# Optimization experiments

Hardware: AMD Instinct MI355X
Metric: run time of the kernel (lower is better)

Reference implementation:

```python
import jax, jax.numpy as jnp
import numpy as np

C = 512
NC = 12
EPS = 1e-5

ADJ = np.array([
    [0,0,0,1,0,1,1,1,1,1,1,1],
    [0,0,0,1,0,1,1,1,1,1,1,1],
    [0,0,0,1,0,1,1,1,1,1,1,1],
    [1,1,1,0,1,1,1,1,1,1,1,1],
    [0,0,0,1,0,1,1,1,1,1,1,1],
    [1,1,1,1,1,0,1,1,1,0,0,0],
    [1,1,1,1,1,1,0,0,0,1,1,1],
    [1,1,1,1,1,1,0,0,0,1,1,1],
    [1,1,1,1,1,1,0,0,0,1,1,1],
    [1,1,1,1,1,0,1,1,1,0,0,0],
    [1,1,1,1,1,0,1,1,1,0,0,0],
    [1,1,1,1,1,0,1,1,1,0,0,0]], dtype=np.float32)
# per-AU region selection: 0=up,1=mid,2=down1,3=down2 (AU1,2,4 up; AU6 mid; AU7 up; AU10 d2; AU12,14,15 d1; AU17,23,24 d2)
SEL = np.array([0,0,0,1,0,3,2,2,2,3,3,3])


def setup_inputs() -> dict:
    key = jax.random.key(0)
    ks = jax.random.split(key, 12)
    B, T = 32, 32
    BT = B * T
    s = (2.0 / C) ** 0.5
    return {
        'x': jax.random.normal(ks[0], (BT, 49, C), jnp.float32),
        'adj_mask': jnp.ones((BT, NC, NC), jnp.float32),
        'region_W': jax.random.normal(ks[1], (4, C, C), jnp.float32) * s,
        'region_b': jnp.zeros((4, C), jnp.float32),
        'region_gamma': jnp.ones((4, C), jnp.float32),
        'region_beta': jnp.zeros((4, C), jnp.float32),
        'upfc_W': jax.random.normal(ks[2], (C, 16), jnp.float32) * 0.02,
        'upfc_b': jnp.zeros((16,), jnp.float32),
        'midfc_W': jax.random.normal(ks[3], (C, 2), jnp.float32) * 0.02,
        'midfc_b': jnp.zeros((2,), jnp.float32),
        'd1fc_W': jax.random.normal(ks[4], (C, 8), jnp.float32) * 0.02,
        'd1fc_b': jnp.zeros((8,), jnp.float32),
        'd2fc_W': jax.random.normal(ks[5], (C, 16), jnp.float32) * 0.02,
        'd2fc_b': jnp.zeros((16,), jnp.float32),
        'class_W': jax.random.normal(ks[6], (NC, C, C), jnp.float32) * s,
        'class_b': jnp.zeros((NC, C), jnp.float32),
        'class_gamma': jnp.ones((NC, C), jnp.float32),
        'class_beta': jnp.zeros((NC, C), jnp.float32),
        'gat_W': jax.random.normal(ks[7], (C, C), jnp.float32) * 0.02,
        'gat_al': jax.random.normal(ks[8], (C,), jnp.float32) * 0.02,
        'gat_ar': jax.random.normal(ks[9], (C,), jnp.float32) * 0.02,
        'tconv_W': jax.random.normal(ks[10], (NC, C, 5), jnp.float32) * 0.1,
        'tconv_b': jnp.zeros((NC, C), jnp.float32),
        'tbn_gamma': jnp.ones((NC,), jnp.float32),
        'tbn_beta': jnp.zeros((NC,), jnp.float32),
        'B': B,
        'T': T,
    }


def _bn(x, gamma, beta, axes):
    # training-mode batch norm: stats over `axes`, affine per remaining channel
    mean = x.mean(axes, keepdims=True)
    var = x.var(axes, keepdims=True)
    return gamma * (x - mean) * jax.lax.rsqrt(var + EPS) + beta


def reference(x, adj_mask, region_W, region_b, region_gamma, region_beta,
              upfc_W, upfc_b, midfc_W, midfc_b, d1fc_W, d1fc_b, d2fc_W, d2fc_b,
              class_W, class_b, class_gamma, class_beta,
              gat_W, gat_al, gat_ar, tconv_W, tconv_b, tbn_gamma, tbn_beta, B, T):
    BT = x.shape[0]
    xg = x.reshape(BT, 7, 7, C)
    x_up = xg[:, :3].reshape(BT, 21, C)
    x_mid = xg[:, 2:5].reshape(BT, 21, C)
    x_down = xg[:, 4:].reshape(BT, 21, C)
    # 4 region LinearBlocks (fc -> BN over (batch,seq) per channel -> relu), batched
    regions = jnp.stack([x_up, x_mid, x_down, x_down])  # [4,BT,21,C]
    h = jnp.einsum('rbsc,rcd->rbsd', regions, region_W) + region_b[:, None, None, :]
    h = jax.nn.relu(_bn(h, region_gamma[:, None, None, :], region_beta[:, None, None, :], (1, 2)))
    up_pred = h[0].mean(1) @ upfc_W + upfc_b
    mid_pred = h[1].mean(1) @ midfc_W + midfc_b
    d1_pred = h[2].mean(1) @ d1fc_W + d1fc_b
    d2_pred = h[3].mean(1) @ d2fc_W + d2fc_b
    # 12 per-AU LinearBlocks, batched over the class dim
    cls_in = h[jnp.asarray(SEL)]  # [12,BT,21,C]
    y = jnp.einsum('nbsc,ncd->nbsd', cls_in, class_W) + class_b[:, None, None, :]
    y = jax.nn.relu(_bn(y, class_gamma[:, None, None, :], class_beta[:, None, None, :], (1, 2)))
    f_v = y.mean(2).transpose(1, 0, 2)  # [BT,12,C]
    # cross-region single-head GAT over the fixed 12-node graph, residual, thred=0.1
    adj = jnp.asarray(ADJ)[None] * adj_mask + jnp.eye(NC, dtype=x.dtype)
    hg = f_v @ gat_W  # [BT,12,C]
    e = jax.nn.leaky_relu((hg @ gat_al)[:, :, None] + (hg @ gat_ar)[:, None, :], 0.2)
    attn = jax.nn.softmax(jnp.where(adj > 0.1, e, -1e9), axis=-1)
    g = jnp.einsum('bij,bjc->bic', attn, hg) + f_v
    # per-class depthwise temporal Conv1d (k=5, pad=2, groups=C), batched over classes
    x4 = g.reshape(B, T, NC, C)
    xp = jnp.pad(x4, ((0, 0), (2, 2), (0, 0), (0, 0)))
    v = sum(xp[:, k:k + T] * tconv_W[None, None, :, :, k] for k in range(5)) + tconv_b[None, None]
    v = v.reshape(BT, NC, C)
    out = jax.nn.relu(_bn(v, tbn_gamma[None, :, None], tbn_beta[None, :, None], (0, 2)))
    return (up_pred, mid_pred, d1_pred, d2_pred, out)
```

## Files before the change

### kernel.cpp

```cpp
#include <hip/hip_runtime.h>
#include <hip/hip_bf16.h>

typedef unsigned short u16;
typedef __attribute__((ext_vector_type(8))) __bf16 bf16x8;
typedef __attribute__((ext_vector_type(8))) u16 u16x8;
typedef __attribute__((ext_vector_type(4))) float floatx4;

#define C_     512
#define NC_    12
#define BT_    1024
#define SEQ_   21
#define M_REG  21504
#define M_GAT  12288

__device__ __forceinline__ float bf2f(u16 u) {
  unsigned int v = ((unsigned int)u) << 16;
  float f; __builtin_memcpy(&f, &v, 4); return f;
}
__device__ __forceinline__ u16 f2bf(float f) {
  unsigned int b; __builtin_memcpy(&b, &f, 4);
  unsigned int r = (b + 0x7FFFu + ((b >> 16) & 1u)) >> 16;
  return (u16)r;
}
__device__ __forceinline__ float ldf(const void* p, size_t i, int f32) {
  return f32 ? ((const float*)p)[i] : bf2f(((const u16*)p)[i]);
}
__device__ __forceinline__ u16 ldbf(const void* p, size_t i, int f32) {
  return f32 ? f2bf(((const float*)p)[i]) : ((const u16*)p)[i];
}
__device__ __forceinline__ void stout(void* p, size_t i, float v, int f32) {
  if (f32) ((float*)p)[i] = v; else ((u16*)p)[i] = f2bf(v);
}

__global__ void sent_k(float* __restrict__ o, float val) {
  const int i = blockIdx.x * 256 + threadIdx.x;
  if (i < 16384) o[i] = val;
}

__global__ void detect_k(const u16* __restrict__ x, int* __restrict__ flag) {
  __shared__ int cnt;
  if (threadIdx.x == 0) cnt = 0;
  __syncthreads();
  int bad = 0;
  for (int i = threadIdx.x; i < 4096; i += 256) {
    const float v = bf2f(x[i]);
    const float a = fabsf(v);
    if (!(a <= 1e4f)) bad++;
    else if (a > 0.f && a < 1e-35f) bad++;
  }
  atomicAdd(&cnt, bad);
  __syncthreads();
  if (threadIdx.x == 0) *flag = (cnt > 400) ? 1 : 0;
}

__global__ void zero_stats(float* __restrict__ p, int n) {
  const int id = blockIdx.x * 256 + threadIdx.x;
  if (id < n) p[id] = 0.f;
}

__global__ void transpose512(const void* __restrict__ rW, const void* __restrict__ cW,
                             const void* __restrict__ gW, u16* __restrict__ oR,
                             u16* __restrict__ oC, u16* __restrict__ oG,
                             const int* __restrict__ flagp) {
  const int f32 = *flagp;
  const int z = blockIdx.z;
  const void* src; u16* dst; size_t sofs = 0;
  if (z < 4)       { src = rW; sofs = (size_t)z*262144;     dst = oR + (size_t)z*262144; }
  else if (z < 16) { src = cW; sofs = (size_t)(z-4)*262144; dst = oC + (size_t)(z-4)*262144; }
  else             { src = gW;                              dst = oG; }
  __shared__ u16 t[32][33];
  const int tx = threadIdx.x;
  const int cy = blockIdx.y * 32, dx = blockIdx.x * 32;
  for (int i = threadIdx.y; i < 32; i += 8)
    t[i][tx] = ldbf(src, sofs + (size_t)(cy + i)*512 + dx + tx, f32);
  __syncthreads();
  for (int i = threadIdx.y; i < 32; i += 8)
    dst[(size_t)(dx + i)*512 + cy + tx] = t[tx][i];
}

template<int MODE>
__global__ __launch_bounds__(256)
void gemm_k(const void* __restrict__ Abase, const u16* __restrict__ Wtb,
            const void* __restrict__ biasb, u16* __restrict__ outb,
            float* __restrict__ ssumb, float* __restrict__ ssqb,
            const int* __restrict__ flagp, int pk, int n0)
{
  const int f32 = *flagp;
  const int z = blockIdx.z;
  const int zeff = (MODE == 1) ? (n0 + z) : z;
  const void* A = Abase;
  if (MODE == 1) A = (const void*)((const u16*)Abase +
        (size_t)((pk >> (zeff * 2)) & 3) * ((size_t)M_REG * C_));
  const u16* Wt = Wtb + (size_t)zeff * C_ * C_;
  u16* Out = outb + (size_t)z * (size_t)M_REG * C_;

  __shared__ __align__(16) u16 As[128*32];
  __shared__ __align__(16) u16 Bs[128*32];

  const int tid  = threadIdx.x;
  const int w    = tid >> 6;
  const int lane = tid & 63;
  const int wm   = w >> 1, wn = w & 1;
  const int r16  = lane & 15, q = lane >> 4;

  const int m0  = blockIdx.y * 128;
  const int nn0 = blockIdx.x * 128;

  const int sub = lane >> 2;
  const int kq  = (lane & 3) * 8;
  const int am0 = m0 + w*32 + sub;
  const int am1 = am0 + 16;
  long ga0, ga1;
  if (MODE == 0) {
    const int roff = (pk >> (z * 8)) & 0xFF;
    int q21 = am0 / 21; int rm = am0 - q21*21;
    ga0 = (long)q21*49 + roff + rm;
    q21 = am1 / 21; rm = am1 - q21*21;
    ga1 = (long)q21*49 + roff + rm;
  } else { ga0 = am0; ga1 = am1; }
  const size_t aOff0 = (size_t)ga0 * C_ + kq;
  const size_t aOff1 = (size_t)ga1 * C_ + kq;
  const u16* bSrc0 = Wt + (size_t)(nn0 + w*32 + sub) * C_ + kq;
  const u16* bSrc1 = bSrc0 + (size_t)16 * C_;
  u16x8* aLds0 = (u16x8*)&As[(w*32 + sub +  0) * 32 + kq];
  u16x8* aLds1 = (u16x8*)&As[(w*32 + sub + 16) * 32 + kq];
  u16x8* bLds0 = (u16x8*)&Bs[(w*32 + sub +  0) * 32 + kq];
  u16x8* bLds1 = (u16x8*)&Bs[(w*32 + sub + 16) * 32 + kq];

  floatx4 acc[4][4];
  #pragma unroll
  for (int i = 0; i < 4; i++)
    #pragma unroll
    for (int j = 0; j < 4; j++)
      acc[i][j] = (floatx4){0.f, 0.f, 0.f, 0.f};

  for (int kk = 0; kk < C_; kk += 32) {
    u16x8 va0, va1;
    if (MODE == 0 && f32) {
      const float* p0 = (const float*)A + aOff0 + kk;
      const float* p1 = (const float*)A + aOff1 + kk;
      const floatx4 f00 = *(const floatx4*)p0;
      const floatx4 f01 = *(const floatx4*)(p0 + 4);
      const floatx4 f10 = *(const floatx4*)p1;
      const floatx4 f11 = *(const floatx4*)(p1 + 4);
      #pragma unroll
      for (int j = 0; j < 4; j++) {
        va0[j] = f2bf(f00[j]); va0[4+j] = f2bf(f01[j]);
        va1[j] = f2bf(f10[j]); va1[4+j] = f2bf(f11[j]);
      }
    } else {
      va0 = *(const u16x8*)((const u16*)A + aOff0 + kk);
      va1 = *(const u16x8*)((const u16*)A + aOff1 + kk);
    }
    const u16x8 vb0 = *(const u16x8*)bSrc0;
    const u16x8 vb1 = *(const u16x8*)bSrc1;
    bSrc0 += 32; bSrc1 += 32;
    __syncthreads();
    *aLds0 = va0; *aLds1 = va1; *bLds0 = vb0; *bLds1 = vb1;
    __syncthreads();
    bf16x8 av[4], bv[4];
    #pragma unroll
    for (int mt = 0; mt < 4; mt++)
      av[mt] = *(const bf16x8*)&As[(wm*64 + mt*16 + r16)*32 + q*8];
    #pragma unroll
    for (int nt = 0; nt < 4; nt++)
      bv[nt] = *(const bf16x8*)&Bs[(wn*64 + nt*16 + r16)*32 + q*8];
    #pragma unroll
    for (int mt = 0; mt < 4; mt++)
      #pragma unroll
      for (int nt = 0; nt < 4; nt++)
        acc[mt][nt] = __builtin_amdgcn_mfma_f32_16x16x32_bf16(av[mt], bv[nt], acc[mt][nt], 0, 0, 0);
  }

  const int colb = nn0 + wn*64;
  const int rowb = m0  + wm*64;
  #pragma unroll
  for (int nt = 0; nt < 4; nt++) {
    const int col = colb + nt*16 + r16;
    float bvv = 0.f;
    if (MODE != 2) bvv = ldf(biasb, (size_t)zeff * C_ + col, f32);
    float s = 0.f, s2 = 0.f;
    #pragma unroll
    for (int mt = 0; mt < 4; mt++) {
      #pragma unroll
      for (int p = 0; p < 4; p++) {
        float v = acc[mt][nt][p] + bvv;
        const int row = rowb + mt*16 + q*4 + p;
        Out[(size_t)row * C_ + col] = f2bf(v);
        s += v; s2 += v*v;
      }
    }
    if (MODE != 2) {
      s  += __shfl_xor(s, 16);  s  += __shfl_xor(s, 32);
      s2 += __shfl_xor(s2, 16); s2 += __shfl_xor(s2, 32);
      if (q == 0) {
        atomicAdd(&ssumb[(size_t)zeff * C_ + col], s);
        atomicAdd(&ssqb [(size_t)zeff * C_ + col], s2);
      }
    }
  }
}

__global__ void bn_region(u16* __restrict__ h, float* __restrict__ hbar,
                          const void* __restrict__ gamma, const void* __restrict__ beta,
                          const float* __restrict__ rsum, const float* __restrict__ rsq,
                          const int* __restrict__ flagp) {
  const int f32 = *flagp;
  const size_t id = (size_t)blockIdx.x * 256 + threadIdx.x;
  const int d  = (int)(id & 511);
  const int bt = (int)((id >> 9) & 1023);
  const int r  = (int)(id >> 19);
  const int rd = r*512 + d;
  const float mean = rsum[rd] * (1.f/21504.f);
  const float var  = fmaxf(rsq[rd] * (1.f/21504.f) - mean*mean, 0.f);
  const float sc = ldf(gamma, rd, f32) * rsqrtf(var + 1e-5f);
  const float sh = ldf(beta, rd, f32) - mean * sc;
  const size_t base = ((size_t)r * M_REG + (size_t)bt * SEQ_) * C_ + d;
  float acc = 0.f;
  #pragma unroll
  for (int s = 0; s < SEQ_; s++) {
    float v = fmaxf(sc * bf2f(h[base + (size_t)s*C_]) + sh, 0.f);
    h[base + (size_t)s*C_] = f2bf(v);
    acc += v;
  }
  hbar[((size_t)r * BT_ + bt) * C_ + d] = acc * (1.f/21.f);
}

__global__ void preds_k(const float* __restrict__ hbar,
                        const void* __restrict__ upW,  const void* __restrict__ upB,
                        const void* __restrict__ midW, const void* __restrict__ midB,
                        const void* __restrict__ d1W,  const void* __restrict__ d1B,
                        const void* __restrict__ d2W,  const void* __restrict__ d2B,
                        void* __restrict__ dout, const int* __restrict__ flagp) {
  const int f32 = *flagp;
  const int bt = blockIdx.x;
  __shared__ float hl[4][512];
  for (int i = threadIdx.x; i < 2048; i += 256)
    hl[i >> 9][i & 511] = hbar[((size_t)(i >> 9) * BT_ + bt) * C_ + (i & 511)];
  __syncthreads();
  const int j = threadIdx.x;
  if (j < 42) {
    int r, wdt, col; const void *W, *Bv; size_t oofs;
    if (j < 16)      { r=0; W=upW;  Bv=upB;  wdt=16; col=j;    oofs = (size_t)bt*16 + col; }
    else if (j < 18) { r=1; W=midW; Bv=midB; wdt=2;  col=j-16; oofs = 16384 + (size_t)bt*2 + col; }
    else if (j < 26) { r=2; W=d1W;  Bv=d1B;  wdt=8;  col=j-18; oofs = 18432 + (size_t)bt*8 + col; }
    else             { r=3; W=d2W;  Bv=d2B;  wdt=16; col=j-26; oofs = 26624 + (size_t)bt*16 + col; }
    float acc = ldf(Bv, col, f32);
    for (int d = 0; d < 512; d++) acc += hl[r][d] * ldf(W, d*wdt + col, f32);
    stout(dout, oofs, acc, f32);
  }
}

__global__ void bn_class_mean(const u16* __restrict__ ypre, u16* __restrict__ fv,
                              const void* __restrict__ gamma, const void* __restrict__ beta,
                              const float* __restrict__ csum, const float* __restrict__ csq,
                              const int* __restrict__ flagp, int n0) {
  const int f32 = *flagp;
  const size_t id = (size_t)blockIdx.x * 256 + threadIdx.x;
  const int d  = (int)(id & 511);
  const int bt = (int)((id >> 9) & 1023);
  const int zz = (int)(id >> 19);
  const int n  = n0 + zz;
  const int nd = n*512 + d;
  const float mean = csum[nd] * (1.f/21504.f);
  const float var  = fmaxf(csq[nd] * (1.f/21504.f) - mean*mean, 0.f);
  const float sc = ldf(gamma, nd, f32) * rsqrtf(var + 1e-5f);
  const float sh = ldf(beta, nd, f32) - mean * sc;
  const size_t base = ((size_t)zz * M_REG + (size_t)bt * SEQ_) * C_ + d;
  float acc = 0.f;
  #pragma unroll
  for (int s = 0; s < SEQ_; s++)
    acc += fmaxf(sc * bf2f(ypre[base + (size_t)s*C_]) + sh, 0.f);
  fv[((size_t)bt * NC_ + n) * C_ + d] = f2bf(acc * (1.f/21.f));
}

__global__ __launch_bounds__(256)
void gat_k(const u16* __restrict__ hg, const u16* __restrict__ fv,
           const void* __restrict__ al, const void* __restrict__ ar,
           const void* __restrict__ adj_mask, float* __restrict__ g,
           const int* __restrict__ flagp) {
  const int f32 = *flagp;
  const int bt = blockIdx.x;
  __shared__ float hl[12][512];
  __shared__ float alv[12], arv[12], attn[12][12];
  const u16* hgb = hg + (size_t)bt * NC_ * C_;
  for (int i = threadIdx.x; i < 6144; i += 256)
    hl[i >> 9][i & 511] = bf2f(hgb[i]);
  __syncthreads();
  const int w = threadIdx.x >> 6, lane = threadIdx.x & 63;
  for (int i = w; i < 12; i += 4) {
    float pa = 0.f, pr = 0.f;
    #pragma unroll
    for (int jj = 0; jj < 8; jj++) {
      const int c = lane*8 + jj;
      const float hv = hl[i][c];
      pa += hv * ldf(al, c, f32);
      pr += hv * ldf(ar, c, f32);
    }
    #pragma unroll
    for (int off = 32; off; off >>= 1) { pa += __shfl_xor(pa, off); pr += __shfl_xor(pr, off); }
    if (lane == 0) { alv[i] = pa; arv[i] = pr; }
  }
  __syncthreads();
  if (threadIdx.x < 12) {
    const unsigned AM[12] = {0xFE8,0xFE8,0xFE8,0xFF7,0xFE8,0x1DF,
                             0xE3F,0xE3F,0xE3F,0x1DF,0x1DF,0x1DF};
    const int i = threadIdx.x;
    float row[12]; float mx = -1e30f;
    #pragma unroll
    for (int jx = 0; jx < 12; jx++) {
      const float maskv = ldf(adj_mask, (size_t)bt*144 + i*12 + jx, f32);
      const float adjv = (float)((AM[i] >> jx) & 1u) * maskv + (i == jx ? 1.f : 0.f);
      float e;
      if (adjv > 0.1f) {
        const float t = alv[i] + arv[jx];
        e = t > 0.f ? t : 0.2f * t;
      } else e = -1e9f;
      row[jx] = e; mx = fmaxf(mx, e);
    }
    float den = 0.f;
    #pragma unroll
    for (int jx = 0; jx < 12; jx++) { const float ex = __expf(row[jx] - mx); row[jx] = ex; den += ex; }
    const float inv = 1.f / den;
    #pragma unroll
    for (int jx = 0; jx < 12; jx++) attn[i][jx] = row[jx] * inv;
  }
  __syncthreads();
  const u16* fvb = fv + (size_t)bt * NC_ * C_;
  float* gb = g + (size_t)bt * NC_ * C_;
  for (int o = threadIdx.x; o < 6144; o += 256) {
    const int i = o >> 9, c = o & 511;
    float acc = bf2f(fvb[o]);
    #pragma unroll
    for (int jx = 0; jx < 12; jx++) acc += attn[i][jx] * hl[jx][c];
    gb[o] = acc;
  }
}

__global__ void tconv_k(float* __restrict__ g, const void* __restrict__ tw,
                        const void* __restrict__ tb, float* __restrict__ tsum,
                        float* __restrict__ tsq, const int* __restrict__ flagp) {
  const int f32 = *flagp;
  const int id = blockIdx.x * 256 + threadIdx.x;
  const int c = id & 511;
  const int n = (id >> 9) % 12;
  const int b = id / 6144;
  float wk[5];
  #pragma unroll
  for (int k = 0; k < 5; k++) wk[k] = ldf(tw, (size_t)(n*512 + c)*5 + k, f32);
  const float bias = ldf(tb, n*512 + c, f32);
  float xv[36];
  xv[0] = xv[1] = xv[34] = xv[35] = 0.f;
  const size_t base = ((size_t)b * 32 * NC_ + n) * C_ + c;
  #pragma unroll
  for (int t = 0; t < 32; t++) xv[t + 2] = g[base + (size_t)t * 6144];
  float s = 0.f, s2 = 0.f;
  float ov[32];
  #pragma unroll
  for (int t = 0; t < 32; t++) {
    float v = bias;
    #pragma unroll
    for (int k = 0; k < 5; k++) v += wk[k] * xv[t + k];
    ov[t] = v; s += v; s2 += v*v;
  }
  #pragma unroll
  for (int t = 0; t < 32; t++) g[base + (size_t)t * 6144] = ov[t];
  #pragma unroll
  for (int off = 32; off; off >>= 1) { s += __shfl_xor(s, off); s2 += __shfl_xor(s2, off); }
  if ((threadIdx.x & 63) == 0) { atomicAdd(&tsum[n], s); atomicAdd(&tsq[n], s2); }
}

__global__ void bn_t(const float* __restrict__ v, void* __restrict__ outp,
                     const void* __restrict__ tg, const void* __restrict__ tb2,
                     const float* __restrict__ tsum, const float* __restrict__ tsq,
                     const int* __restrict__ flagp) {
  const int f32 = *flagp;
  const size_t id = (size_t)blockIdx.x * 256 + threadIdx.x;
  const int n = (int)((id >> 9) % 12);
  const float mean = tsum[n] * (1.f/524288.f);
  const float var  = fmaxf(tsq[n] * (1.f/524288.f) - mean*mean, 0.f);
  const float sc = ldf(tg, n, f32) * rsqrtf(var + 1e-5f);
  const float sh = ldf(tb2, n, f32) - mean * sc;
  stout(outp, 43008 + id, fmaxf(sc * v[id] + sh, 0.f), f32);
}

static constexpr size_t OFF_FLAG = 0;
static constexpr size_t OFF_STAT = 64;
static constexpr int    STAT_N   = 2048+2048+6144+6144+12+12;
static constexpr size_t OFF_WTR  = 65792;
static constexpr size_t OFF_WTC  = OFF_WTR + (size_t)4*512*512*2;
static constexpr size_t OFF_WTG  = OFF_WTC + (size_t)12*512*512*2;
static constexpr size_t OFF_H    = OFF_WTG + (size_t)512*512*2;
static constexpr size_t OFF_HBAR = OFF_H + (size_t)4*M_REG*C_*2;
static constexpr size_t OFF_FV   = OFF_HBAR + (size_t)4*BT_*C_*4;
static constexpr size_t OFF_AREN = OFF_FV + (size_t)M_GAT*C_*2;
static constexpr size_t YPRE_B   = (size_t)M_REG * C_ * 2;
static constexpr size_t NEEDED   = OFF_AREN + YPRE_B;

extern "C" void kernel_launch(void* const* d_in, const int* in_sizes, int n_in,
                              void* d_out, int out_size, void* d_ws, size_t ws_size,
                              hipStream_t stream) {
  const u16* x        = (const u16*)d_in[0];
  const void* adj_m   = d_in[1];
  const void* region_W= d_in[2];
  const void* region_b= d_in[3];
  const void* region_g= d_in[4];
  const void* region_be=d_in[5];
  const void* upW  = d_in[6];   const void* upB  = d_in[7];
  const void* midW = d_in[8];   const void* midB = d_in[9];
  const void* d1W  = d_in[10];  const void* d1B  = d_in[11];
  const void* d2W  = d_in[12];  const void* d2B  = d_in[13];
  const void* class_W = d_in[14];
  const void* class_b = d_in[15];
  const void* class_g = d_in[16];
  const void* class_be= d_in[17];
  const void* gat_W   = d_in[18];
  const void* gat_al  = d_in[19];
  const void* gat_ar  = d_in[20];
  const void* tconv_W = d_in[21];
  const void* tconv_b = d_in[22];
  const void* tbn_g   = d_in[23];
  const void* tbn_be  = d_in[24];

  char* ws = (char*)d_ws;
  int*   flagp = (int*)(ws + OFF_FLAG);
  float* rsum = (float*)(ws + OFF_STAT);
  float* rsq  = rsum + 2048;
  float* csum = rsq  + 2048;
  float* csq  = csum + 6144;
  float* tsum = csq  + 6144;
  float* tsq  = tsum + 12;
  u16*   WtR  = (u16*)(ws + OFF_WTR);
  u16*   WtC  = (u16*)(ws + OFF_WTC);
  u16*   WtG  = (u16*)(ws + OFF_WTG);
  u16*   h    = (u16*)(ws + OFF_H);
  float* hbar = (float*)(ws + OFF_HBAR);
  u16*   fv   = (u16*)(ws + OFF_FV);
  u16*   ypre = (u16*)(ws + OFF_AREN);
  u16*   hg   = (u16*)(ws + OFF_AREN);
  float* g    = (float*)(ws + OFF_H);

  int errStage = 0, errCode = 0;
  (void)hipGetLastError();
  #define CK(s) do { hipError_t e_ = hipGetLastError(); \
      if (e_ != hipSuccess && errStage == 0) { errStage = (s); errCode = (int)e_; } } while(0)

  sent_k<<<64, 256, 0, stream>>>((float*)d_out, 50.f); CK(12);

  if (ws_size < NEEDED) {
    int mb = (int)(ws_size >> 20); if (mb > 999) mb = 999;
    sent_k<<<64, 256, 0, stream>>>((float*)d_out, 13000.f + (float)mb);
    return;
  }

  int nch = (int)((ws_size - OFF_AREN) / YPRE_B);
  if (nch > 12) nch = 12;
  if (nch < 1) nch = 1;

  const int ROFFPACK = 0 | (14 << 8) | (28 << 16) | (28 << 24);
  const int SELPACK  = (1 << 6) | (3 << 10) | (2 << 12) | (2 << 14) |
                       (2 << 16) | (3 << 18) | (3 << 20) | (3 << 22);

  detect_k<<<1, 256, 0, stream>>>(x, flagp);                         CK(1);
  zero_stats<<<(STAT_N + 255)/256, 256, 0, stream>>>(rsum, STAT_N);  CK(1);
  transpose512<<<dim3(16,16,17), dim3(32,8), 0, stream>>>(
      region_W, class_W, gat_W, WtR, WtC, WtG, flagp);               CK(2);

  gemm_k<0><<<dim3(4,168,4), 256, 0, stream>>>(
      x, WtR, region_b, h, rsum, rsq, flagp, ROFFPACK, 0);           CK(3);
  bn_region<<<8192, 256, 0, stream>>>(h, hbar, region_g, region_be,
      rsum, rsq, flagp);                                             CK(4);
  preds_k<<<1024, 256, 0, stream>>>(hbar, upW,upB, midW,midB,
      d1W,d1B, d2W,d2B, d_out, flagp);                               CK(5);

  for (int n0 = 0; n0 < 12; n0 += nch) {
    const int zc = (12 - n0) < nch ? (12 - n0) : nch;
    gemm_k<1><<<dim3(4,168,zc), 256, 0, stream>>>(
        h, WtC - (size_t)n0*262144 + (size_t)n0*262144, class_b, ypre,
        csum, csq, flagp, SELPACK, n0);                              CK(6);
    bn_class_mean<<<zc*2048, 256, 0, stream>>>(ypre, fv, class_g, class_be,
        csum, csq, flagp, n0);                                       CK(7);
  }

  gemm_k<2><<<dim3(4,96,1), 256, 0, stream>>>(
      fv, WtG, nullptr, hg, nullptr, nullptr, flagp, 0, 0);          CK(8);
  gat_k<<<1024, 256, 0, stream>>>(hg, fv, gat_al, gat_ar, adj_m, g, flagp); CK(9);
  tconv_k<<<768, 256, 0, stream>>>(g, tconv_W, tconv_b, tsum, tsq, flagp);  CK(10);
  bn_t<<<24576, 256, 0, stream>>>(g, d_out, tbn_g, tbn_be, tsum, tsq, flagp); CK(11);

  if (errStage) {
    int ec = errCode > 999 ? 999 : errCode;
    sent_k<<<64, 256, 0, stream>>>((float*)d_out, (float)(errStage*1000 + ec));
  }
  #undef CK
}
```

Measured before the change: 894.1 us.

## Use direct global-to-LDS loads in GEMM and vectorize BN reduction kernels

The GEMM tile loads now use global_load_lds to copy A and B tiles straight into shared memory instead of staging them through registers. The f32 path keeps its register conversion for A and uses the direct path only for B. The bn_region and bn_class_mean kernels now have each lane handle 8 contiguous channels with 16-byte vector loads and stores, using one-eighth as many blocks. This cuts register traffic and instruction count in memory-bound kernels. The risk is that the LDS layout written by global_load_lds must match the old per-lane write pattern, and per-thread register use rises in the BN kernels.

```diff
diff --git a/kernel.cpp b/kernel.cpp
--- a/kernel.cpp
+++ b/kernel.cpp
@@ -30,6 +30,12 @@
 }
 __device__ __forceinline__ void stout(void* p, size_t i, float v, int f32) {
   if (f32) ((float*)p)[i] = v; else ((u16*)p)[i] = f2bf(v);
+}
+
+typedef __attribute__((address_space(1))) unsigned int as1_u32;
+typedef __attribute__((address_space(3))) unsigned int as3_u32;
+__device__ __forceinline__ void gl2lds16(const void* g, void* l) {
+  __builtin_amdgcn_global_load_lds((const as1_u32*)g, (as3_u32*)l, 16, 0, 0);
 }
 
 __global__ void sent_k(float* __restrict__ o, float val) {
@@ -122,10 +128,12 @@
   const size_t aOff1 = (size_t)ga1 * C_ + kq;
   const u16* bSrc0 = Wt + (size_t)(nn0 + w*32 + sub) * C_ + kq;
   const u16* bSrc1 = bSrc0 + (size_t)16 * C_;
+  u16* aDstW0 = &As[(w*32 +  0) * 32];
+  u16* aDstW1 = &As[(w*32 + 16) * 32];
+  u16* bDstW0 = &Bs[(w*32 +  0) * 32];
+  u16* bDstW1 = &Bs[(w*32 + 16) * 32];
   u16x8* aLds0 = (u16x8*)&As[(w*32 + sub +  0) * 32 + kq];
   u16x8* aLds1 = (u16x8*)&As[(w*32 + sub + 16) * 32 + kq];
-  u16x8* bLds0 = (u16x8*)&Bs[(w*32 + sub +  0) * 32 + kq];
-  u16x8* bLds1 = (u16x8*)&Bs[(w*32 + sub + 16) * 32 + kq];
 
   floatx4 acc[4][4];
   #pragma unroll
@@ -135,7 +143,6 @@
       acc[i][j] = (floatx4){0.f, 0.f, 0.f, 0.f};
 
   for (int kk = 0; kk < C_; kk += 32) {
-    u16x8 va0, va1;
     if (MODE == 0 && f32) {
       const float* p0 = (const float*)A + aOff0 + kk;
       const float* p1 = (const float*)A + aOff1 + kk;
@@ -143,21 +150,25 @@
       const floatx4 f01 = *(const floatx4*)(p0 + 4);
       const floatx4 f10 = *(const floatx4*)p1;
       const floatx4 f11 = *(const floatx4*)(p1 + 4);
+      u16x8 va0, va1;
       #pragma unroll
       for (int j = 0; j < 4; j++) {
         va0[j] = f2bf(f00[j]); va0[4+j] = f2bf(f01[j]);
         va1[j] = f2bf(f10[j]); va1[4+j] = f2bf(f11[j]);
       }
+      __syncthreads();
+      gl2lds16(bSrc0, bDstW0); gl2lds16(bSrc1, bDstW1);
+      *aLds0 = va0; *aLds1 = va1;
+      __syncthreads();
     } else {
-      va0 = *(const u16x8*)((const u16*)A + aOff0 + kk);
-      va1 = *(const u16x8*)((const u16*)A + aOff1 + kk);
+      __syncthreads();
+      gl2lds16((const u16*)A + aOff0 + kk, aDstW0);
+      gl2lds16((const u16*)A + aOff1 + kk, aDstW1);
+      gl2lds16(bSrc0, bDstW0);
+      gl2lds16(bSrc1, bDstW1);
+      __syncthreads();
     }
-    const u16x8 vb0 = *(const u16x8*)bSrc0;
-    const u16x8 vb1 = *(const u16x8*)bSrc1;
     bSrc0 += 32; bSrc1 += 32;
-    __syncthreads();
-    *aLds0 = va0; *aLds1 = va1; *bLds0 = vb0; *bLds1 = vb1;
-    __syncthreads();
     bf16x8 av[4], bv[4];
     #pragma unroll
     for (int mt = 0; mt < 4; mt++)
@@ -206,24 +217,36 @@
                           const float* __restrict__ rsum, const float* __restrict__ rsq,
                           const int* __restrict__ flagp) {
   const int f32 = *flagp;
-  const size_t id = (size_t)blockIdx.x * 256 + threadIdx.x;
-  const int d  = (int)(id & 511);
-  const int bt = (int)((id >> 9) & 1023);
-  const int r  = (int)(id >> 19);
-  const int rd = r*512 + d;
-  const float mean = rsum[rd] * (1.f/21504.f);
-  const float var  = fmaxf(rsq[rd] * (1.f/21504.f) - mean*mean, 0.f);
-  const float sc = ldf(gamma, rd, f32) * rsqrtf(var + 1e-5f);
-  const float sh = ldf(beta, rd, f32) - mean * sc;
-  const size_t base = ((size_t)r * M_REG + (size_t)bt * SEQ_) * C_ + d;
-  float acc = 0.f;
+  const int gid  = blockIdx.x;
+  const int r    = gid >> 8;
+  const int bt   = ((gid & 255) << 2) + (threadIdx.x >> 6);
+  const int lane = threadIdx.x & 63;
+  const int d0   = lane * 8;
+  const int rd   = r*512 + d0;
+  float sc[8], sh[8], accv[8];
+  #pragma unroll
+  for (int j = 0; j < 8; j++) {
+    const float mean = rsum[rd+j] * (1.f/21504.f);
+    const float var  = fmaxf(rsq[rd+j] * (1.f/21504.f) - mean*mean, 0.f);
+    sc[j] = ldf(gamma, rd+j, f32) * rsqrtf(var + 1e-5f);
+    sh[j] = ldf(beta,  rd+j, f32) - mean * sc[j];
+    accv[j] = 0.f;
+  }
+  const size_t base = ((size_t)r * M_REG + (size_t)bt * SEQ_) * C_ + d0;
   #pragma unroll
   for (int s = 0; s < SEQ_; s++) {
-    float v = fmaxf(sc * bf2f(h[base + (size_t)s*C_]) + sh, 0.f);
-    h[base + (size_t)s*C_] = f2bf(v);
-    acc += v;
-  }
-  hbar[((size_t)r * BT_ + bt) * C_ + d] = acc * (1.f/21.f);
+    u16x8 vv = *(u16x8*)&h[base + (size_t)s*C_];
+    #pragma unroll
+    for (int j = 0; j < 8; j++) {
+      float v = fmaxf(sc[j] * bf2f(vv[j]) + sh[j], 0.f);
+      vv[j] = f2bf(v);
+      accv[j] += v;
+    }
+    *(u16x8*)&h[base + (size_t)s*C_] = vv;
+  }
+  float* hb = &hbar[((size_t)r * BT_ + bt) * C_ + d0];
+  #pragma unroll
+  for (int j = 0; j < 8; j++) hb[j] = accv[j] * (1.f/21.f);
 }
 
 __global__ void preds_k(const float* __restrict__ hbar,
@@ -256,22 +279,34 @@
                               const float* __restrict__ csum, const float* __restrict__ csq,
                               const int* __restrict__ flagp, int n0) {
   const int f32 = *flagp;
-  const size_t id = (size_t)blockIdx.x * 256 + threadIdx.x;
-  const int d  = (int)(id & 511);
-  const int bt = (int)((id >> 9) & 1023);
-  const int zz = (int)(id >> 19);
-  const int n  = n0 + zz;
-  const int nd = n*512 + d;
-  const float mean = csum[nd] * (1.f/21504.f);
-  const float var  = fmaxf(csq[nd] * (1.f/21504.f) - mean*mean, 0.f);
-  const float sc = ldf(gamma, nd, f32) * rsqrtf(var + 1e-5f);
-  const float sh = ldf(beta, nd, f32) - mean * sc;
-  const size_t base = ((size_t)zz * M_REG + (size_t)bt * SEQ_) * C_ + d;
-  float acc = 0.f;
-  #pragma unroll
-  for (int s = 0; s < SEQ_; s++)
-    acc += fmaxf(sc * bf2f(ypre[base + (size_t)s*C_]) + sh, 0.f);
-  fv[((size_t)bt * NC_ + n) * C_ + d] = f2bf(acc * (1.f/21.f));
+  const int gid  = blockIdx.x;
+  const int zz   = gid >> 8;
+  const int bt   = ((gid & 255) << 2) + (threadIdx.x >> 6);
+  const int lane = threadIdx.x & 63;
+  const int d0   = lane * 8;
+  const int n    = n0 + zz;
+  const int nd   = n*512 + d0;
+  float sc[8], sh[8], accv[8];
+  #pragma unroll
+  for (int j = 0; j < 8; j++) {
+    const float mean = csum[nd+j] * (1.f/21504.f);
+    const float var  = fmaxf(csq[nd+j] * (1.f/21504.f) - mean*mean, 0.f);
+    sc[j] = ldf(gamma, nd+j, f32) * rsqrtf(var + 1e-5f);
+    sh[j] = ldf(beta,  nd+j, f32) - mean * sc[j];
+    accv[j] = 0.f;
+  }
+  const size_t base = ((size_t)zz * M_REG + (size_t)bt * SEQ_) * C_ + d0;
+  #pragma unroll
+  for (int s = 0; s < SEQ_; s++) {
+    const u16x8 vv = *(const u16x8*)&ypre[base + (size_t)s*C_];
+    #pragma unroll
+    for (int j = 0; j < 8; j++)
+      accv[j] += fmaxf(sc[j] * bf2f(vv[j]) + sh[j], 0.f);
+  }
+  u16x8 ov;
+  #pragma unroll
+  for (int j = 0; j < 8; j++) ov[j] = f2bf(accv[j] * (1.f/21.f));
+  *(u16x8*)&fv[((size_t)bt * NC_ + n) * C_ + d0] = ov;
 }
 
 __global__ __launch_bounds__(256)
@@ -468,7 +503,7 @@
 
   gemm_k<0><<<dim3(4,168,4), 256, 0, stream>>>(
       x, WtR, region_b, h, rsum, rsq, flagp, ROFFPACK, 0);           CK(3);
-  bn_region<<<8192, 256, 0, stream>>>(h, hbar, region_g, region_be,
+  bn_region<<<1024, 256, 0, stream>>>(h, hbar, region_g, region_be,
       rsum, rsq, flagp);                                             CK(4);
   preds_k<<<1024, 256, 0, stream>>>(hbar, upW,upB, midW,midB,
       d1W,d1B, d2W,d2B, d_out, flagp);                               CK(5);
@@ -476,9 +511,8 @@
   for (int n0 = 0; n0 < 12; n0 += nch) {
     const int zc = (12 - n0) < nch ? (12 - n0) : nch;
     gemm_k<1><<<dim3(4,168,zc), 256, 0, stream>>>(
-        h, WtC - (size_t)n0*262144 + (size_t)n0*262144, class_b, ypre,
-        csum, csq, flagp, SELPACK, n0);                              CK(6);
-    bn_class_mean<<<zc*2048, 256, 0, stream>>>(ypre, fv, class_g, class_be,
+        h, WtC, class_b, ypre, csum, csq, flagp, SELPACK, n0);       CK(6);
+    bn_class_mean<<<zc*256, 256, 0, stream>>>(ypre, fv, class_g, class_be,
         csum, csq, flagp, n0);                                       CK(7);
   }
 
```

Measured after the change: 860.4 us. 3.8% less time.
